# Optimization experiments

Hardware: AMD Instinct MI355X
Metric: run time of the kernel (lower is better)

Reference implementation:

```python
import jax, jax.numpy as jnp
import numpy as np

B, H, LQ, LV, D = 32, 8, 256, 1024, 512


def setup_inputs() -> dict:
    key = jax.random.key(0)
    ks = jax.random.split(key, 10)
    sc = 0.02
    return {
        "queries": jax.random.normal(ks[0], (B, H, LQ, D), jnp.float32),
        "keys": jax.random.normal(ks[1], (B, LV, D), jnp.float32),
        "values": jax.random.normal(ks[2], (B, LV, D), jnp.float32),
        "W_q": sc * jax.random.normal(ks[3], (D, D), jnp.float32),
        "W_k": sc * jax.random.normal(ks[4], (D, D), jnp.float32),
        "W_v": sc * jax.random.normal(ks[5], (D, D), jnp.float32),
        "W_o": sc * jax.random.normal(ks[6], (D, D), jnp.float32),
        "W_len": sc * jax.random.normal(ks[7], (LQ, LV), jnp.float32),
        "b_len": sc * jax.random.normal(ks[8], (LQ,), jnp.float32),
        "valid_lens": jax.random.randint(ks[9], (B,), 0, LQ).astype(jnp.int32),
    }


def _multi_len_att(x, W_len, b_len):
    # x: [B, LV, D]; torch does permute(0,2,1) then Linear(LV->LQ) then
    # permute back; the identical linear is repeated per head (broadcast).
    # result per head: [B, LQ, D]
    return jnp.einsum('bld,ql->bqd', x, W_len) + b_len[None, :, None]


def reference(queries, keys, values, W_q, W_k, W_v, W_o, W_len, b_len, valid_lens):
    # queries: [B, H, LQ, D] -> W_q -> merge batch/head
    q = jnp.einsum('bhqd,ed->bhqe', queries, W_q).reshape(B * H, LQ, D)
    # keys/values: length-projection (shared across heads), then W_k/W_v
    k1 = jnp.einsum('bqd,ed->bqe', _multi_len_att(keys, W_len, b_len), W_k)   # [B, LQ, D]
    v1 = jnp.einsum('bqd,ed->bqe', _multi_len_att(values, W_len, b_len), W_v)  # [B, LQ, D]
    k = jnp.broadcast_to(k1[:, None], (B, H, LQ, D)).reshape(B * H, LQ, D)
    v = jnp.broadcast_to(v1[:, None], (B, H, LQ, D)).reshape(B * H, LQ, D)
    # scaled dot-product attention with valid-length masking
    scores = jnp.einsum('nqd,nkd->nqk', q, k) / jnp.sqrt(jnp.float32(D))  # [B*H, LQ, LQ]
    vl = jnp.repeat(valid_lens, H)                                        # [B*H]
    mask = jnp.arange(LQ)[None, None, :] < vl[:, None, None]
    scores = jnp.where(mask, scores, jnp.float32(-1e6))
    attn = jax.nn.softmax(scores, axis=-1)
    out = jnp.einsum('nqk,nkd->nqd', attn, v).reshape(B, H, LQ, D)
    return jnp.einsum('bhqd,ed->bhqe', out, W_o)
```

## Files before the change

kernel.cpp:

```cpp
#include <hip/hip_runtime.h>
#include <math.h>

#define Bc  32
#define Hc  8
#define LQc 256
#define LVc 1024
#define Dc  512

#define VMCNT0 asm volatile("s_waitcnt vmcnt(0)" ::: "memory")
#define VMCNT(N) asm volatile("s_waitcnt vmcnt(" #N ")" ::: "memory")

typedef short bf16x8 __attribute__((ext_vector_type(8)));
typedef float f32x4  __attribute__((ext_vector_type(4)));

__device__ __forceinline__ unsigned short f2bf(float x) {
    unsigned u = __builtin_bit_cast(unsigned, x);
    u = (u + 0x7fffu + ((u >> 16) & 1u)) >> 16;
    return (unsigned short)u;
}

__device__ __forceinline__ bf16x8 pack8(float4 a, float4 b) {
    bf16x8 r;
    r[0] = (short)f2bf(a.x); r[1] = (short)f2bf(a.y);
    r[2] = (short)f2bf(a.z); r[3] = (short)f2bf(a.w);
    r[4] = (short)f2bf(b.x); r[5] = (short)f2bf(b.y);
    r[6] = (short)f2bf(b.z); r[7] = (short)f2bf(b.w);
    return r;
}

__device__ __forceinline__ void gload16(const ushort* g, ushort* l) {
    __builtin_amdgcn_global_load_lds(
        (const __attribute__((address_space(1))) unsigned*)g,
        (__attribute__((address_space(3))) unsigned*)l, 16, 0, 0);
}

__global__ __launch_bounds__(256) void prep_w(const float* __restrict__ Wq,
                                              const float* __restrict__ Wk,
                                              const float* __restrict__ Wv,
                                              const float* __restrict__ Wo,
                                              const float* __restrict__ Wl,
                                              ushort* __restrict__ wqT,
                                              ushort* __restrict__ wkT,
                                              ushort* __restrict__ wvT,
                                              ushort* __restrict__ woBf,
                                              ushort* __restrict__ wlBf) {
    const int z = blockIdx.z;
    if (z < 3) {
        __shared__ float t[32][33];
        const float* in = (z == 0) ? Wq : (z == 1) ? Wk : Wv;
        ushort* out = (z == 0) ? wqT : (z == 1) ? wkT : wvT;
        const int l0 = blockIdx.x * 32, d0 = blockIdx.y * 32;
        const int r = threadIdx.x >> 5, c = threadIdx.x & 31;
#pragma unroll
        for (int i = 0; i < 4; i++)
            t[r + 8 * i][c] = in[(size_t)(l0 + r + 8 * i) * 512 + d0 + c];
        __syncthreads();
#pragma unroll
        for (int i = 0; i < 4; i++)
            out[(size_t)(d0 + r + 8 * i) * 512 + l0 + c] = f2bf(t[c][r + 8 * i]);
    } else {
        const float* in = (z == 3) ? Wo : Wl;
        ushort* out = (z == 3) ? woBf : wlBf;
        const int i = (blockIdx.y * 16 + blockIdx.x) * 256 + threadIdx.x;
        float4 v = ((const float4*)in)[i];
        ushort4 o;
        o.x = f2bf(v.x); o.y = f2bf(v.y); o.z = f2bf(v.z); o.w = f2bf(v.w);
        ((ushort4*)out)[i] = o;
    }
}

__global__ __launch_bounds__(256) void lenproj_f32(const ushort* __restrict__ wl,
                                                   const float* __restrict__ keys,
                                                   const float* __restrict__ vals,
                                                   const float* __restrict__ bias,
                                                   ushort* __restrict__ t1k) {
    __shared__ __align__(16) ushort Wls[4096];
    __shared__ __align__(16) float  Xsf[128 * 36];

    const int z = blockIdx.z;
    const float* X = ((z < 32) ? keys : vals) + (size_t)(z & 31) * LVc * Dc;
    ushort* C = t1k + (size_t)z * LQc * Dc;

    const int bm = blockIdx.y * 128;
    const int bn = blockIdx.x * 128;
    const int tid = threadIdx.x;
    const int wave = tid >> 6, l = tid & 63;
    const int wm = (wave >> 1) * 64, wn = (wave & 1) * 64;
    const int l15 = l & 15, lh = l >> 4;

    f32x4 acc[4][4];
#pragma unroll
    for (int m = 0; m < 4; m++)
#pragma unroll
        for (int n = 0; n < 4; n++) acc[m][n] = (f32x4){0.f, 0.f, 0.f, 0.f};

    const int lrow = tid >> 3;
    const int dcol = (tid & 7) * 16;

    for (int l0 = 0; l0 < LVc; l0 += 32) {
        gload16(wl + (size_t)(bm + wave * 16 + l15) * LVc + l0 + lh * 8,
                Wls + wave * 512);
        gload16(wl + (size_t)(bm + 64 + wave * 16 + l15) * LVc + l0 + lh * 8,
                Wls + (wave + 4) * 512);
        const float* xs = X + (size_t)(l0 + lrow) * Dc + bn + dcol;
        float4 xv0 = ((const float4*)xs)[0];
        float4 xv1 = ((const float4*)xs)[1];
        float4 xv2 = ((const float4*)xs)[2];
        float4 xv3 = ((const float4*)xs)[3];
        Xsf[(dcol + 0)  * 36 + lrow] = xv0.x;
        Xsf[(dcol + 1)  * 36 + lrow] = xv0.y;
        Xsf[(dcol + 2)  * 36 + lrow] = xv0.z;
        Xsf[(dcol + 3)  * 36 + lrow] = xv0.w;
        Xsf[(dcol + 4)  * 36 + lrow] = xv1.x;
        Xsf[(dcol + 5)  * 36 + lrow] = xv1.y;
        Xsf[(dcol + 6)  * 36 + lrow] = xv1.z;
        Xsf[(dcol + 7)  * 36 + lrow] = xv1.w;
        Xsf[(dcol + 8)  * 36 + lrow] = xv2.x;
        Xsf[(dcol + 9)  * 36 + lrow] = xv2.y;
        Xsf[(dcol + 10) * 36 + lrow] = xv2.z;
        Xsf[(dcol + 11) * 36 + lrow] = xv2.w;
        Xsf[(dcol + 12) * 36 + lrow] = xv3.x;
        Xsf[(dcol + 13) * 36 + lrow] = xv3.y;
        Xsf[(dcol + 14) * 36 + lrow] = xv3.z;
        Xsf[(dcol + 15) * 36 + lrow] = xv3.w;
        VMCNT0;
        __syncthreads();

        bf16x8 af[4], bfr[4];
#pragma unroll
        for (int m = 0; m < 4; m++)
            af[m] = *(const bf16x8*)&Wls[((wm >> 4) + m) * 512 + lh * 128 + l15 * 8];
#pragma unroll
        for (int n = 0; n < 4; n++) {
            const float* fb = &Xsf[(wn + n * 16 + l15) * 36 + lh * 8];
            float4 x0 = *(const float4*)fb;
            float4 x1 = *(const float4*)(fb + 4);
            bfr[n] = pack8(x0, x1);
        }
#pragma unroll
        for (int m = 0; m < 4; m++)
#pragma unroll
            for (int n = 0; n < 4; n++)
                acc[m][n] = __builtin_amdgcn_mfma_f32_16x16x32_bf16(
                    af[m], bfr[n], acc[m][n], 0, 0, 0);
        __syncthreads();
    }

#pragma unroll
    for (int m = 0; m < 4; m++)
#pragma unroll
        for (int r = 0; r < 4; r++) {
            const int row = bm + wm + m * 16 + lh * 4 + r;
            const float bv = bias[row];
#pragma unroll
            for (int n = 0; n < 4; n++) {
                const int col = bn + wn + n * 16 + l15;
                C[(size_t)row * Dc + col] = f2bf(acc[m][n][r] + bv);
            }
        }
}

template <int STORE, bool BIAS, int SWIZ>
__global__ __launch_bounds__(256) void gemm_bt(const ushort* __restrict__ A,
                                               const ushort* __restrict__ B,
                                               void* __restrict__ Cv,
                                               const float* __restrict__ bias,
                                               int M, int N, int K, float alpha,
                                               long sA, long sB, long sC,
                                               int byPerXcd) {
    __shared__ ushort As[128 * 32];
    __shared__ ushort Bs[128 * 32];
    const int z = blockIdx.z;
    A += (size_t)z * sA;
    B += (size_t)z * sB;
    float*  Cf = (float*)Cv  + (size_t)z * sC;
    ushort* Ch = (ushort*)Cv + (size_t)z * sC;

    int bm, bn;
    if constexpr (SWIZ) {
        const int bid = blockIdx.x;
        const int xcd = bid & 7, slot = bid >> 3;
        bm = (xcd * byPerXcd + (slot >> 2)) * 128;
        bn = (slot & 3) * 128;
    } else {
        bm = blockIdx.y * 128;
        bn = blockIdx.x * 128;
    }
    const int tid = threadIdx.x;
    const int wave = tid >> 6, l = tid & 63;
    const int wm = (wave >> 1) * 64, wn = (wave & 1) * 64;
    const int l15 = l & 15, lh = l >> 4;

    f32x4 acc[4][4];
#pragma unroll
    for (int m = 0; m < 4; m++)
#pragma unroll
        for (int n = 0; n < 4; n++) acc[m][n] = (f32x4){0.f, 0.f, 0.f, 0.f};

    const int srow = tid >> 2, scol = (tid & 3) * 8;
    ushort* ldsA = As + (wave * 16) * 32;
    ushort* ldsB = Bs + (wave * 16) * 32;
    const ushort* gA = A + (size_t)(bm + srow) * K + scol;
    const ushort* gB = B + (size_t)(bn + srow) * K + scol;

    for (int k0 = 0; k0 < K; k0 += 32) {
        gload16(gA + k0, ldsA);
        gload16(gA + k0 + (size_t)64 * K, ldsA + 64 * 32);
        gload16(gB + k0, ldsB);
        gload16(gB + k0 + (size_t)64 * K, ldsB + 64 * 32);
        VMCNT0;
        __syncthreads();
        bf16x8 af[4], bfr[4];
#pragma unroll
        for (int m = 0; m < 4; m++)
            af[m] = *(const bf16x8*)&As[(wm + m * 16 + l15) * 32 + lh * 8];
#pragma unroll
        for (int n = 0; n < 4; n++)
            bfr[n] = *(const bf16x8*)&Bs[(wn + n * 16 + l15) * 32 + lh * 8];
#pragma unroll
        for (int m = 0; m < 4; m++)
#pragma unroll
            for (int n = 0; n < 4; n++)
                acc[m][n] = __builtin_amdgcn_mfma_f32_16x16x32_bf16(
                    af[m], bfr[n], acc[m][n], 0, 0, 0);
        __syncthreads();
    }

    if constexpr (STORE == 2) {
#pragma unroll
        for (int m = 0; m < 4; m++) {
            const int row0 = bm + wm + m * 16 + lh * 4;
            const int bb = row0 >> 8, q = row0 & 255;
            float bv[4] = {0.f, 0.f, 0.f, 0.f};
            if constexpr (BIAS) {
#pragma unroll
                for (int r = 0; r < 4; r++) bv[r] = bias[q + r];
            }
#pragma unroll
            for (int n = 0; n < 4; n++) {
                const int col = bn + wn + n * 16 + l15;
                ushort4 o;
                o.x = f2bf(acc[m][n][0] * alpha + bv[0]);
                o.y = f2bf(acc[m][n][1] * alpha + bv[1]);
                o.z = f2bf(acc[m][n][2] * alpha + bv[2]);
                o.w = f2bf(acc[m][n][3] * alpha + bv[3]);
                *(ushort4*)&Ch[(size_t)bb * N * 256 + (size_t)col * 256 + q] = o;
            }
        }
    } else if constexpr (STORE == 1) {
#pragma unroll
        for (int m = 0; m < 4; m++)
#pragma unroll
            for (int r = 0; r < 4; r++) {
                const int row = bm + wm + m * 16 + lh * 4 + r;
                const float bv = BIAS ? bias[row & 255] : 0.f;
#pragma unroll
                for (int n = 0; n < 4; n++) {
                    const int col = bn + wn + n * 16 + l15;
                    Ch[(size_t)row * N + col] = f2bf(acc[m][n][r] * alpha + bv);
                }
            }
    } else {
#pragma unroll
        for (int m = 0; m < 4; m++)
#pragma unroll
            for (int r = 0; r < 4; r++) {
                const int row = bm + wm + m * 16 + lh * 4 + r;
                const float bv = BIAS ? bias[row & 255] : 0.f;
#pragma unroll
                for (int n = 0; n < 4; n++) {
                    const int col = bn + wn + n * 16 + l15;
                    Cf[(size_t)row * N + col] = acc[m][n][r] * alpha + bv;
                }
            }
    }
}

__global__ __launch_bounds__(512, 2) void attn_mfma(const float* __restrict__ qf,
                                                    const ushort* __restrict__ k2,
                                                    const ushort* __restrict__ v2T,
                                                    const int* __restrict__ vlen,
                                                    float* __restrict__ aout) {
    __shared__ __align__(16) ushort pool[40960];
    ushort* Ps = pool;

    const int bid = blockIdx.x;
    const int xcd = bid & 7, pos = bid >> 3;
    const int b = xcd * 4 + (pos >> 4);
    const int inner = pos & 15;
    const int h = inner >> 1, qh = inner & 1;
    const int n = b * 8 + h;
    const int q0 = qh * 128;

    const int tid = threadIdx.x, wave = tid >> 6, l = tid & 63;
    const int l15 = l & 15, lh = l >> 4;
    const int vl = vlen[b];

    const float*  qbase = qf  + ((size_t)n * LQc + q0) * Dc;
    const ushort* kbase = k2  + (size_t)b * LQc * Dc;
    const ushort* vbase = v2T + (size_t)b * LQc * Dc;

    f32x4 sacc[16];
#pragma unroll
    for (int fn = 0; fn < 16; fn++) sacc[fn] = (f32x4){0.f, 0.f, 0.f, 0.f};

    auto STAGE_K = [&](int bi, int k0) {
        ushort* k_ = pool + bi * 16384;
#pragma unroll
        for (int j = 0; j < 2; j++) {
            const int g = wave * 2 + j;
            gload16(kbase + (size_t)(g * 16 + l15) * Dc + k0 + lh * 8,
                    k_ + g * 1024);
            gload16(kbase + (size_t)(g * 16 + l15) * Dc + k0 + 32 + lh * 8,
                    k_ + g * 1024 + 512);
        }
    };

    STAGE_K(0, 0);
    VMCNT0;
    __syncthreads();
    for (int t = 0; t < 8; ++t) {
        const int k0 = t * 64;
        if (t < 7) STAGE_K((t + 1) & 1, k0 + 64);
        const ushort* k_ = pool + (t & 1) * 16384;
#pragma unroll
        for (int s = 0; s < 2; ++s) {
            const float* fb = qbase + (size_t)(wave * 16 + l15) * Dc + k0 + s * 32 + lh * 8;
            float4 x0 = *(const float4*)fb;
            float4 x1 = *(const float4*)(fb + 4);
            bf16x8 aq = pack8(x0, x1);
#pragma unroll
            for (int fn = 0; fn < 16; fn++) {
                bf16x8 bk = *(const bf16x8*)&k_[fn * 1024 + s * 512 + lh * 128 + l15 * 8];
                sacc[fn] = __builtin_amdgcn_mfma_f32_16x16x32_bf16(aq, bk, sacc[fn], 0, 0, 0);
            }
        }
        VMCNT0;
        __syncthreads();
    }

    auto STAGE_V = [&](int bi, int it) {
        const int d0 = (it >> 3) * 128, l0 = (it & 7) * 32;
        ushort* v_ = pool + 32768 + bi * 4096;
        gload16(vbase + (size_t)(d0 + wave * 16 + l15) * LQc + l0 + lh * 8,
                v_ + wave * 512);
    };
    STAGE_V(0, 0);

#pragma unroll
    for (int r = 0; r < 4; r++) {
        const int rowl = wave * 16 + lh * 4 + r;
        float v[16];
        float rmax = -3.4e38f;
#pragma unroll
        for (int fn = 0; fn < 16; fn++) {
            const int col = fn * 16 + l15;
            float s = sacc[fn][r];
            v[fn] = (col < vl) ? s : -1e6f;
            rmax = fmaxf(rmax, v[fn]);
        }
        rmax = fmaxf(rmax, __shfl_xor(rmax, 1));
        rmax = fmaxf(rmax, __shfl_xor(rmax, 2));
        rmax = fmaxf(rmax, __shfl_xor(rmax, 4));
        rmax = fmaxf(rmax, __shfl_xor(rmax, 8));
        float rsum = 0.f;
#pragma unroll
        for (int fn = 0; fn < 16; fn++) {
            v[fn] = __expf(v[fn] - rmax);
            rsum += v[fn];
        }
        rsum += __shfl_xor(rsum, 1);
        rsum += __shfl_xor(rsum, 2);
        rsum += __shfl_xor(rsum, 4);
        rsum += __shfl_xor(rsum, 8);
        const float rinv = 1.0f / rsum;
        const int base = wave * 4096 + (lh * 4 + r) * 8 + (l15 & 7);
        const int chi = (l15 >> 3) * 128;
#pragma unroll
        for (int fn = 0; fn < 16; fn++)
            Ps[base + fn * 256 + chi] = f2bf(v[fn] * rinv);
    }
    VMCNT0;
    __syncthreads();

    int it = 0;
    for (int d0 = 0; d0 < Dc; d0 += 128) {
        f32x4 o[8];
#pragma unroll
        for (int qf2 = 0; qf2 < 8; qf2++) o[qf2] = (f32x4){0.f, 0.f, 0.f, 0.f};

        for (int l0 = 0; l0 < LQc; l0 += 32, ++it) {
            if (it < 31) {
                STAGE_V((it + 1) & 1, it + 1);
                VMCNT(1);
            } else {
                VMCNT0;
            }
            const ushort* v_ = pool + 32768 + (it & 1) * 4096;
            bf16x8 vb = *(const bf16x8*)&v_[wave * 512 + lh * 128 + l15 * 8];
            const int pcol = (l0 >> 3) + lh;
#pragma unroll
            for (int qf2 = 0; qf2 < 8; qf2++) {
                bf16x8 pa = *(const bf16x8*)&Ps[qf2 * 4096 + pcol * 128 + l15 * 8];
                o[qf2] = __builtin_amdgcn_mfma_f32_16x16x32_bf16(pa, vb, o[qf2], 0, 0, 0);
            }
        }
#pragma unroll
        for (int qf2 = 0; qf2 < 8; qf2++)
#pragma unroll
            for (int r = 0; r < 4; r++) {
                const int rowl = qf2 * 16 + lh * 4 + r;
                const int col = d0 + wave * 16 + l15;
                aout[((size_t)n * LQc + q0 + rowl) * Dc + col] = o[qf2][r];
            }
    }
}

extern "C" void kernel_launch(void* const* d_in, const int* in_sizes, int n_in,
                              void* d_out, int out_size, void* d_ws, size_t ws_size,
                              hipStream_t stream) {
    const float* queries    = (const float*)d_in[0];
    const float* keys       = (const float*)d_in[1];
    const float* values     = (const float*)d_in[2];
    const float* W_q        = (const float*)d_in[3];
    const float* W_k        = (const float*)d_in[4];
    const float* W_v        = (const float*)d_in[5];
    const float* W_o        = (const float*)d_in[6];
    const float* W_len      = (const float*)d_in[7];
    const float* b_len      = (const float*)d_in[8];
    const int*   valid_lens = (const int*)d_in[9];

    char* ws = (char*)d_ws;
    const size_t MB = 1024 * 1024;
    ushort* wqT  = (ushort*)(ws + 128 * MB);
    ushort* woBf = wqT  + 262144;
    ushort* wkT  = woBf + 262144;
    ushort* wvT  = wkT  + 262144;
    ushort* Eq   = wvT  + 262144;
    ushort* G    = Eq   + 262144;
    ushort* wl   = G    + 262144;
    ushort* t1k  = wl   + 262144;
    ushort* t1v  = t1k  + 4194304;
    ushort* k2   = t1v  + 4194304;
    ushort* v2T  = k2   + 4194304;

    const float alpha_q = 0.044194173824159216f;
    dim3 blk(256);

    prep_w<<<dim3(16, 16, 5), blk, 0, stream>>>(W_q, W_k, W_v, W_o, W_len,
                                                wqT, wkT, wvT, woBf, wl);
    gemm_bt<1, false, 0><<<dim3(4, 4, 2), blk, 0, stream>>>(
        wqT, wkT, Eq, nullptr, 512, 512, 512, 1.f, 262144, 262144, 262144, 0);

    lenproj_f32<<<dim3(4, 2, 64), blk, 0, stream>>>(wl, keys, values, b_len, t1k);

    gemm_bt<1, false, 1><<<dim3(256), blk, 0, stream>>>(
        t1k, Eq, k2, nullptr, 8192, 512, 512, alpha_q, 0, 0, 0, 8);
    gemm_bt<2, false, 1><<<dim3(256), blk, 0, stream>>>(
        t1v, G, v2T, nullptr, 8192, 512, 512, 1.f, 0, 0, 0, 8);

    attn_mfma<<<dim3(512), dim3(512), 0, stream>>>(queries, k2, v2T, valid_lens,
                                                   (float*)d_out);
}
```

Measured before the change: 203.6 us.

## Triple-buffer K tiles with prefetched Q registers in score GEMM

```diff
diff --git a/kernel.cpp b/kernel.cpp
--- a/kernel.cpp
+++ b/kernel.cpp
@@ -9,6 +9,7 @@
 
 #define VMCNT0 asm volatile("s_waitcnt vmcnt(0)" ::: "memory")
 #define VMCNT(N) asm volatile("s_waitcnt vmcnt(" #N ")" ::: "memory")
+#define SCHEDB __builtin_amdgcn_sched_barrier(0)
 
 typedef short bf16x8 __attribute__((ext_vector_type(8)));
 typedef float f32x4  __attribute__((ext_vector_type(4)));
@@ -305,37 +306,45 @@
     for (int fn = 0; fn < 16; fn++) sacc[fn] = (f32x4){0.f, 0.f, 0.f, 0.f};
 
     auto STAGE_K = [&](int bi, int k0) {
-        ushort* k_ = pool + bi * 16384;
+        ushort* k_ = pool + bi * 8192;
 #pragma unroll
         for (int j = 0; j < 2; j++) {
             const int g = wave * 2 + j;
             gload16(kbase + (size_t)(g * 16 + l15) * Dc + k0 + lh * 8,
-                    k_ + g * 1024);
-            gload16(kbase + (size_t)(g * 16 + l15) * Dc + k0 + 32 + lh * 8,
-                    k_ + g * 1024 + 512);
+                    k_ + g * 512);
         }
     };
-
+    auto QL = [&](int k0, float4* q) {
+        const float* fb = qbase + (size_t)(wave * 16 + l15) * Dc + k0 + lh * 8;
+        q[0] = *(const float4*)fb;
+        q[1] = *(const float4*)(fb + 4);
+    };
+
+    float4 qr[2][2];
     STAGE_K(0, 0);
-    VMCNT0;
+    STAGE_K(1, 32);
+    SCHEDB;
+    QL(0, qr[0]);
+    VMCNT(4);
+    SCHEDB;
     __syncthreads();
-    for (int t = 0; t < 8; ++t) {
-        const int k0 = t * 64;
-        if (t < 7) STAGE_K((t + 1) & 1, k0 + 64);
-        const ushort* k_ = pool + (t & 1) * 16384;
-#pragma unroll
-        for (int s = 0; s < 2; ++s) {
-            const float* fb = qbase + (size_t)(wave * 16 + l15) * Dc + k0 + s * 32 + lh * 8;
-            float4 x0 = *(const float4*)fb;
-            float4 x1 = *(const float4*)(fb + 4);
-            bf16x8 aq = pack8(x0, x1);
-#pragma unroll
-            for (int fn = 0; fn < 16; fn++) {
-                bf16x8 bk = *(const bf16x8*)&k_[fn * 1024 + s * 512 + lh * 128 + l15 * 8];
-                sacc[fn] = __builtin_amdgcn_mfma_f32_16x16x32_bf16(aq, bk, sacc[fn], 0, 0, 0);
-            }
-        }
-        VMCNT0;
+
+#pragma unroll
+    for (int t = 0; t < 16; ++t) {
+        if (t + 2 < 16) STAGE_K((t + 2) % 3, (t + 2) * 32);
+        SCHEDB;
+        if (t + 1 < 16) QL((t + 1) * 32, qr[(t + 1) & 1]);
+        if (t < 14)      { VMCNT(4); }
+        else if (t == 14){ VMCNT(2); }
+        else             { VMCNT(0); }
+        SCHEDB;
+        bf16x8 aq = pack8(qr[t & 1][0], qr[t & 1][1]);
+        const ushort* k_ = pool + (t % 3) * 8192;
+#pragma unroll
+        for (int fn = 0; fn < 16; fn++) {
+            bf16x8 bk = *(const bf16x8*)&k_[fn * 512 + lh * 128 + l15 * 8];
+            sacc[fn] = __builtin_amdgcn_mfma_f32_16x16x32_bf16(aq, bk, sacc[fn], 0, 0, 0);
+        }
         __syncthreads();
     }
 
@@ -396,6 +405,7 @@
             } else {
                 VMCNT0;
             }
+            SCHEDB;
             const ushort* v_ = pool + 32768 + (it & 1) * 4096;
             bf16x8 vb = *(const bf16x8*)&v_[wave * 512 + lh * 128 + l15 * 8];
             const int pcol = (l0 >> 3) + lh;
```

After: 203.6 us (median of 2 runs). About the same (-0.0%).
